# Performance work log

Measured on AMD Instinct MI355X. Metric: run time of the kernel, lower is better.

## Reference

```python
import jax, jax.numpy as jnp
import numpy as np

WS = 8          # window size
HEADS = 6
DIM = 192


def _rel_idx(ws):
    # index [q, k] -> flat relative-position index into table of size (2ws-1)^2
    pos = jnp.arange(ws * ws)
    ph, pw = pos // ws, pos % ws
    rel_h = ph[None, :] - ph[:, None] + ws - 1  # k_h - q_h + ws - 1
    rel_w = pw[None, :] - pw[:, None] + ws - 1
    return rel_h * (2 * ws - 1) + rel_w  # [ws*ws, ws*ws]


def setup_inputs() -> dict:
    key = jax.random.key(0)
    ks = jax.random.split(key, 4)
    x = jax.random.normal(ks[0], (4, DIM, 256, 256), jnp.float32)
    qkv_w = jax.random.normal(ks[1], (3 * DIM, DIM), jnp.float32) * 0.02  # 1x1 conv
    qkv_b = jnp.zeros((3 * DIM,), jnp.float32)
    out_w = jax.random.normal(ks[2], (DIM, DIM), jnp.float32) * 0.02      # 1x1 conv
    out_b = jnp.zeros((DIM,), jnp.float32)
    rpe_table = jax.random.normal(ks[3], (HEADS, (2 * WS - 1) ** 2), jnp.float32) * 0.001
    return {"x": x, "qkv_w": qkv_w, "qkv_b": qkv_b,
            "out_w": out_w, "out_b": out_b, "rpe_table": rpe_table}


def reference(x, qkv_w, qkv_b, out_w, out_b, rpe_table):
    B, C, H, W = x.shape
    ws, heads = WS, HEADS
    hd, wd = H // ws, W // ws          # H,W chosen divisible by ws -> pad is no-op
    c = C // heads                     # head dim
    n = ws * ws                        # tokens per window

    # 1x1 conv to qkv
    qkv = jnp.einsum('bchw,oc->bohw', x, qkv_w) + qkv_b[None, :, None, None]
    # feat_to_win: b (3 heads c) (hd ws) (wd ws) -> 3, (b hd wd), heads, n, c
    qkv = qkv.reshape(B, 3, heads, c, hd, ws, wd, ws)
    qkv = qkv.transpose(1, 0, 4, 6, 2, 5, 7, 3).reshape(3, B * hd * wd, heads, n, c)
    q, k, v = qkv[0], qkv[1], qkv[2]

    bias = rpe_table[:, _rel_idx(ws)]  # [heads, n, n]
    scale = c ** -0.5
    scores = jnp.einsum('whqc,whkc->whqk', q, k) * scale + bias[None]
    attn = jax.nn.softmax(scores, axis=-1)
    out = jnp.einsum('whqk,whkc->whqc', attn, v)

    # win_to_feat: (b hd wd) heads n c -> b (heads c) H W
    out = out.reshape(B, hd, wd, heads, ws, ws, c)
    out = out.transpose(0, 3, 6, 1, 4, 2, 5).reshape(B, C, H, W)

    out = jnp.einsum('bchw,oc->bohw', out, out_w) + out_b[None, :, None, None]
    return out
```

## Files before the change

### kernel.cpp

```cpp
#include <hip/hip_runtime.h>
#include <cstdint>
#include <cstddef>

typedef __attribute__((ext_vector_type(8))) short short8;
typedef __attribute__((ext_vector_type(4))) float floatx4;

#define SEG 50331648ull

__device__ __forceinline__ unsigned short bf16rne(float f) {
  union { float f; unsigned int u; } c; c.f = f;
  unsigned int u = c.u;
  return (unsigned short)((u + 0x7fffu + ((u >> 16) & 1u)) >> 16);
}
__device__ __forceinline__ unsigned int packbf(float a, float b) {
  return (unsigned int)bf16rne(a) | ((unsigned int)bf16rne(b) << 16);
}

__global__ __launch_bounds__(256) void x_to_bf16(const float* __restrict__ x,
                                                 unsigned short* __restrict__ xb) {
  __shared__ float Tl[64][65];
  const int tid = threadIdx.x;
  const int ptile = blockIdx.x, cc = blockIdx.y, b = blockIdx.z;
  const float* src = x + ((size_t)(b * 192 + cc * 64)) * 65536 + ptile * 64;
  {
    int row = tid >> 2;
    int cb = (tid & 3) * 4;
#pragma unroll
    for (int rr = 0; rr < 4; ++rr) {
      int col = cb + rr * 16;
      float4 v = *(const float4*)(src + (size_t)row * 65536 + col);
      *(float4*)&Tl[row][col] = v;
    }
  }
  __syncthreads();
  unsigned short* dst = xb + ((size_t)b * 65536 + (size_t)ptile * 64) * 192 + cc * 64;
  {
    int p_l = tid >> 2;
    int c0 = (tid & 3) * 16;
    unsigned int w[8];
#pragma unroll
    for (int e = 0; e < 8; ++e)
      w[e] = packbf(Tl[c0 + 2 * e][p_l], Tl[c0 + 2 * e + 1][p_l]);
    *(uint4*)(dst + (size_t)p_l * 192 + c0)     = make_uint4(w[0], w[1], w[2], w[3]);
    *(uint4*)(dst + (size_t)p_l * 192 + c0 + 8) = make_uint4(w[4], w[5], w[6], w[7]);
  }
}

__global__ void bias_prep(const float* __restrict__ rpe, float* __restrict__ bias_d) {
  const int head = blockIdx.x;
  const int tid = threadIdx.x;
  for (int e = tid; e < 1024; e += 256) {
    int it = e >> 8, jt = (e >> 6) & 3, ln = e & 63;
    int quad = ln >> 4, n = ln & 15;
    int j = jt * 16 + n;
    int jh = j >> 3, jw = j & 7;
    float4 out;
    float* o = (float*)&out;
#pragma unroll
    for (int r = 0; r < 4; ++r) {
      int m = it * 16 + quad * 4 + r;
      int idx = (jh - (m >> 3) + 7) * 15 + (jw - (m & 7) + 7);
      o[r] = rpe[head * 225 + idx];
    }
    *(float4*)(bias_d + ((size_t)(head * 16 + it * 4 + jt) * 64 + ln) * 4) = out;
  }
}

#define WP 200
#define XP 200
__global__ __launch_bounds__(256) void qkv_mm(
    const unsigned short* __restrict__ xb, const float* __restrict__ wq,
    const float* __restrict__ qkv_b,
    unsigned short* __restrict__ q, unsigned short* __restrict__ k,
    unsigned short* __restrict__ v) {
  __shared__ unsigned short Xl[128 * XP];
  __shared__ unsigned short Wl[64 * WP];
  const int tid = threadIdx.x;
  const int pt = blockIdx.x, b = blockIdx.y;
  const int lane = tid & 63, w = tid >> 6;
  const int n16 = lane & 15, quad = lane >> 4;

  const unsigned short* xrow = xb + ((size_t)b * 65536 + (size_t)pt * 128) * 192;
#pragma unroll
  for (int r = 0; r < 12; ++r) {
    int c = tid + 256 * r;
    int row = c / 24;
    int col = (c - row * 24) * 8;
    short8 xv = *(const short8*)(xrow + (size_t)c * 8);
    *(short8*)&Xl[row * XP + col] = xv;
  }
  const int wo = tid >> 2, wcb = (tid & 3) * 4;
  float4 wpre[12];
#pragma unroll
  for (int r = 0; r < 12; ++r)
    wpre[r] = *(const float4*)(wq + (size_t)wo * 192 + wcb + r * 16);
#pragma unroll
  for (int r = 0; r < 12; ++r)
    *(uint2*)&Wl[wo * WP + wcb + r * 16] =
        make_uint2(packbf(wpre[r].x, wpre[r].y), packbf(wpre[r].z, wpre[r].w));
  __syncthreads();

  const floatx4 fz = {0.f, 0.f, 0.f, 0.f};
#pragma unroll 1
  for (int ot = 0; ot < 9; ++ot) {
    if (ot < 8) {
      const float* wr = wq + (size_t)((ot + 1) * 64 + wo) * 192 + wcb;
#pragma unroll
      for (int r = 0; r < 12; ++r) wpre[r] = *(const float4*)(wr + r * 16);
    }
    floatx4 acc[4][2];
#pragma unroll
    for (int i = 0; i < 4; ++i)
#pragma unroll
      for (int j = 0; j < 2; ++j) acc[i][j] = fz;
#pragma unroll
    for (int k0 = 0; k0 < 192; k0 += 32) {
      short8 a[4], bf[2];
#pragma unroll
      for (int i = 0; i < 4; ++i)
        a[i] = *(const short8*)&Wl[(16 * i + n16) * WP + k0 + quad * 8];
#pragma unroll
      for (int j = 0; j < 2; ++j)
        bf[j] = *(const short8*)&Xl[(w * 32 + 16 * j + n16) * XP + k0 + quad * 8];
#pragma unroll
      for (int i = 0; i < 4; ++i)
#pragma unroll
        for (int j = 0; j < 2; ++j)
          acc[i][j] = __builtin_amdgcn_mfma_f32_16x16x32_bf16(a[i], bf[j], acc[i][j], 0, 0, 0);
    }
    __syncthreads();
    if (ot < 8) {
#pragma unroll
      for (int r = 0; r < 12; ++r)
        *(uint2*)&Wl[wo * WP + wcb + r * 16] =
            make_uint2(packbf(wpre[r].x, wpre[r].y), packbf(wpre[r].z, wpre[r].w));
    }
    __syncthreads();

    const int sel = ot / 3;
    unsigned short* dst = (sel == 0) ? q : ((sel == 1) ? k : v);
    const float scl = (sel == 0) ? 0.17677669529663687f : 1.0f;
    const int h = pt >> 1;
#pragma unroll
    for (int j = 0; j < 2; ++j) {
      int wcol = w * 32 + 16 * j + n16;
      int wc = ((pt & 1) << 7) + wcol;
      int win = (b << 10) + (h >> 3) * 32 + (wc >> 3);
      int t = ((h & 7) << 3) + (wc & 7);
#pragma unroll
      for (int i = 0; i < 4; ++i) {
        int og = ot * 64 + 16 * i + quad * 4;
        int off = og - sel * 192;
        int head = off >> 5, c = off & 31;
        float4 bb = *(const float4*)(qkv_b + og);
        float v0 = (acc[i][j][0] + bb.x) * scl;
        float v1 = (acc[i][j][1] + bb.y) * scl;
        float v2 = (acc[i][j][2] + bb.z) * scl;
        float v3 = (acc[i][j][3] + bb.w) * scl;
        *(uint2*)(dst + ((size_t)(win * 6 + head) * 64 + t) * 32 + c) =
            make_uint2(packbf(v0, v1), packbf(v2, v3));
      }
    }
  }
}

__global__ __launch_bounds__(256) void attn(
    const unsigned short* __restrict__ q, const unsigned short* __restrict__ k,
    const unsigned short* __restrict__ v, const float* __restrict__ bias_d,
    unsigned short* __restrict__ AO) {
  __shared__ unsigned short pl[4][64 * 72];
  __shared__ unsigned short vl[4][32 * 72];
  const int tid = threadIdx.x, w = tid >> 6, lane = tid & 63;
  const int n16 = lane & 15, quad = lane >> 4;
  const int wh = blockIdx.x * 4 + w;
  const int win = wh / 6, head = wh - win * 6;
  const unsigned short* qb = q + (size_t)wh * 2048;
  const unsigned short* kb = k + (size_t)wh * 2048;
  const unsigned short* vb = v + (size_t)wh * 2048;

  short8 vrow[4];
#pragma unroll
  for (int c8 = 0; c8 < 4; ++c8)
    vrow[c8] = *(const short8*)(vb + lane * 32 + c8 * 8);

  short8 aq[4], bk[4];
#pragma unroll
  for (int it = 0; it < 4; ++it)
    aq[it] = *(const short8*)(qb + (16 * it + n16) * 32 + quad * 8);
#pragma unroll
  for (int jt = 0; jt < 4; ++jt)
    bk[jt] = *(const short8*)(kb + (16 * jt + n16) * 32 + quad * 8);

  unsigned short* vlw = (unsigned short*)vl[w];
#pragma unroll
  for (int c8 = 0; c8 < 4; ++c8)
#pragma unroll
    for (int e = 0; e < 8; ++e)
      vlw[(c8 * 8 + e) * 72 + lane] = (unsigned short)vrow[c8][e];

  floatx4 s[4][4];
  const floatx4 fz = {0.f, 0.f, 0.f, 0.f};
#pragma unroll
  for (int it = 0; it < 4; ++it)
#pragma unroll
    for (int jt = 0; jt < 4; ++jt)
      s[it][jt] = __builtin_amdgcn_mfma_f32_16x16x32_bf16(aq[it], bk[jt], fz, 0, 0, 0);

  const float* bD = bias_d + (size_t)head * 4096;
  unsigned short* plw = (unsigned short*)pl[w];
#pragma unroll
  for (int it = 0; it < 4; ++it) {
    floatx4 bb[4];
#pragma unroll
    for (int jt = 0; jt < 4; ++jt)
      bb[jt] = *(const floatx4*)(bD + ((size_t)(it * 4 + jt) * 64 + lane) * 4);
#pragma unroll
    for (int r = 0; r < 4; ++r) {
      float x0 = s[it][0][r] + bb[0][r];
      float x1 = s[it][1][r] + bb[1][r];
      float x2 = s[it][2][r] + bb[2][r];
      float x3 = s[it][3][r] + bb[3][r];
      float m = fmaxf(fmaxf(x0, x1), fmaxf(x2, x3));
      m = fmaxf(m, __shfl_xor(m, 1));
      m = fmaxf(m, __shfl_xor(m, 2));
      m = fmaxf(m, __shfl_xor(m, 4));
      m = fmaxf(m, __shfl_xor(m, 8));
      float e0 = __expf(x0 - m), e1 = __expf(x1 - m);
      float e2 = __expf(x2 - m), e3 = __expf(x3 - m);
      float sum = e0 + e1 + e2 + e3;
      sum += __shfl_xor(sum, 1);
      sum += __shfl_xor(sum, 2);
      sum += __shfl_xor(sum, 4);
      sum += __shfl_xor(sum, 8);
      float inv = 1.0f / sum;
      int mr = it * 16 + quad * 4 + r;
      plw[mr * 72 + 0 * 16 + n16] = bf16rne(e0 * inv);
      plw[mr * 72 + 1 * 16 + n16] = bf16rne(e1 * inv);
      plw[mr * 72 + 2 * 16 + n16] = bf16rne(e2 * inv);
      plw[mr * 72 + 3 * 16 + n16] = bf16rne(e3 * inv);
    }
  }

  short8 bv[2][2], ap[4][2];
#pragma unroll
  for (int ct = 0; ct < 2; ++ct)
#pragma unroll
    for (int kk = 0; kk < 2; ++kk)
      bv[ct][kk] = *(const short8*)&vlw[(16 * ct + n16) * 72 + kk * 32 + quad * 8];
#pragma unroll
  for (int it = 0; it < 4; ++it)
#pragma unroll
    for (int kk = 0; kk < 2; ++kk)
      ap[it][kk] = *(const short8*)&plw[(16 * it + n16) * 72 + kk * 32 + quad * 8];
  floatx4 o[4][2];
#pragma unroll
  for (int it = 0; it < 4; ++it)
#pragma unroll
    for (int ct = 0; ct < 2; ++ct) {
      floatx4 acc = __builtin_amdgcn_mfma_f32_16x16x32_bf16(ap[it][0], bv[ct][0], fz, 0, 0, 0);
      o[it][ct] = __builtin_amdgcn_mfma_f32_16x16x32_bf16(ap[it][1], bv[ct][1], acc, 0, 0, 0);
    }

  unsigned short* ol = plw;
#pragma unroll
  for (int it = 0; it < 4; ++it)
#pragma unroll
    for (int ct = 0; ct < 2; ++ct)
#pragma unroll
      for (int r = 0; r < 4; ++r)
        ol[(16 * it + quad * 4 + r) * 40 + 16 * ct + n16] = bf16rne(o[it][ct][r]);

  const int t = lane;
  const int bimg = win >> 10, rem = win & 1023;
  const int h0 = (rem >> 5) << 3, w0 = (rem & 31) << 3;
  const size_t pix = ((size_t)bimg << 16) + (size_t)(h0 + (t >> 3)) * 256 + w0 + (t & 7);
  unsigned short* dstp = AO + pix * 192 + head * 32;
#pragma unroll
  for (int c8 = 0; c8 < 4; ++c8)
    *(short8*)(dstp + c8 * 8) = *(const short8*)&ol[t * 40 + c8 * 8];
}

__global__ __launch_bounds__(256) void out_mm(
    const unsigned short* __restrict__ AO, const float* __restrict__ w2,
    const float* __restrict__ b2, float* __restrict__ out) {
  __shared__ unsigned short Xl[128 * XP];
  __shared__ unsigned short Wl[64 * WP];
  const int tid = threadIdx.x;
  const int pt = blockIdx.x, b = blockIdx.y;
  const int lane = tid & 63, w = tid >> 6;
  const int n16 = lane & 15, quad = lane >> 4;

  const unsigned short* arow = AO + ((size_t)b * 65536 + (size_t)pt * 128) * 192;
#pragma unroll
  for (int r = 0; r < 12; ++r) {
    int c = tid + 256 * r;
    int row = c / 24;
    int col = (c - row * 24) * 8;
    short8 xv = *(const short8*)(arow + (size_t)c * 8);
    *(short8*)&Xl[row * XP + col] = xv;
  }
  const int wo = tid >> 2, wcb = (tid & 3) * 4;
  float4 wpre[12];
#pragma unroll
  for (int r = 0; r < 12; ++r)
    wpre[r] = *(const float4*)(w2 + (size_t)wo * 192 + wcb + r * 16);
#pragma unroll
  for (int r = 0; r < 12; ++r)
    *(uint2*)&Wl[wo * WP + wcb + r * 16] =
        make_uint2(packbf(wpre[r].x, wpre[r].y), packbf(wpre[r].z, wpre[r].w));
  __syncthreads();

  const floatx4 fz = {0.f, 0.f, 0.f, 0.f};
#pragma unroll 1
  for (int ot = 0; ot < 3; ++ot) {
    if (ot < 2) {
      const float* wr = w2 + (size_t)((ot + 1) * 64 + wo) * 192 + wcb;
#pragma unroll
      for (int r = 0; r < 12; ++r) wpre[r] = *(const float4*)(wr + r * 16);
    }
    floatx4 acc[2][4];
#pragma unroll
    for (int i = 0; i < 2; ++i)
#pragma unroll
      for (int j = 0; j < 4; ++j) acc[i][j] = fz;
#pragma unroll
    for (int k0 = 0; k0 < 192; k0 += 32) {
      short8 a[2], bf[4];
#pragma unroll
      for (int i = 0; i < 2; ++i)
        a[i] = *(const short8*)&Xl[(w * 32 + 16 * i + n16) * XP + k0 + quad * 8];
#pragma unroll
      for (int j = 0; j < 4; ++j)
        bf[j] = *(const short8*)&Wl[(16 * j + n16) * WP + k0 + quad * 8];
#pragma unroll
      for (int i = 0; i < 2; ++i)
#pragma unroll
        for (int j = 0; j < 4; ++j)
          acc[i][j] = __builtin_amdgcn_mfma_f32_16x16x32_bf16(a[i], bf[j], acc[i][j], 0, 0, 0);
    }
    __syncthreads();
    if (ot < 2) {
#pragma unroll
      for (int r = 0; r < 12; ++r)
        *(uint2*)&Wl[wo * WP + wcb + r * 16] =
            make_uint2(packbf(wpre[r].x, wpre[r].y), packbf(wpre[r].z, wpre[r].w));
    }
    __syncthreads();

#pragma unroll
    for (int j = 0; j < 4; ++j) {
      int o = ot * 64 + 16 * j + n16;
      float bj = b2[o];
      float* obase = out + ((size_t)b * 192 + o) * 65536 + (size_t)pt * 128;
#pragma unroll
      for (int i = 0; i < 2; ++i) {
        int p = w * 32 + 16 * i + quad * 4;
        *(float4*)(obase + p) = make_float4(acc[i][j][0] + bj, acc[i][j][1] + bj,
                                            acc[i][j][2] + bj, acc[i][j][3] + bj);
      }
    }
  }
}

extern "C" void kernel_launch(void* const* d_in, const int* in_sizes, int n_in,
                              void* d_out, int out_size, void* d_ws, size_t ws_size,
                              hipStream_t stream) {
  const float* x     = (const float*)d_in[0];
  const float* qkv_w = (const float*)d_in[1];
  const float* qkv_b = (const float*)d_in[2];
  const float* out_w = (const float*)d_in[3];
  const float* out_b = (const float*)d_in[4];
  const float* rpe   = (const float*)d_in[5];
  float* out = (float*)d_out;

  unsigned short* xb = (unsigned short*)d_ws;
  unsigned short* q  = xb + SEG;
  unsigned short* k  = q + SEG;
  unsigned short* v  = k + SEG;
  unsigned short* AO = v + SEG;
  float* bias_d = (float*)(AO + SEG);

  x_to_bf16<<<dim3(1024, 3, 4), 256, 0, stream>>>(x, xb);
  bias_prep<<<6, 256, 0, stream>>>(rpe, bias_d);
  qkv_mm<<<dim3(512, 4), 256, 0, stream>>>(xb, qkv_w, qkv_b, q, k, v);
  attn<<<6144, 256, 0, stream>>>(q, k, v, bias_d, AO);
  out_mm<<<dim3(512, 4), 256, 0, stream>>>(AO, out_w, out_b, out);
}
```

Before: 678.5 us.

## Rework attention kernel with 32x32 MFMA transposed scores and register-resident softmax

Rewrites the per-window attention kernel to compute S^T with 32x32x16 bf16 MFMAs, so each lane holds a full query column and softmax needs only one cross-half shuffle. Probabilities are packed to bf16 in registers and rearranged with permlane32 swaps to feed the PV MFMA directly. This removes the P round trip through LDS and the output staging buffer. Normalisation is deferred to the output, and the bias table layout is regenerated to match the new fragment layout. Output stores become narrower scattered 8-byte writes instead of 16-byte rows.

Measured after the change: 666.7 us. Within noise of the previous version (-1.7%).

```diff
diff --git a/kernel.cpp b/kernel.cpp
--- a/kernel.cpp
+++ b/kernel.cpp
@@ -4,6 +4,7 @@
 
 typedef __attribute__((ext_vector_type(8))) short short8;
 typedef __attribute__((ext_vector_type(4))) float floatx4;
+typedef __attribute__((ext_vector_type(16))) float floatx16;
 
 #define SEG 50331648ull
 
@@ -14,6 +15,11 @@
 }
 __device__ __forceinline__ unsigned int packbf(float a, float b) {
   return (unsigned int)bf16rne(a) | ((unsigned int)bf16rne(b) << 16);
+}
+__device__ __forceinline__ unsigned int cvtpk(float lo, float hi) {
+  unsigned int r;
+  asm("v_cvt_pk_bf16_f32 %0, %1, %2" : "=v"(r) : "v"(lo), "v"(hi));
+  return r;
 }
 
 __global__ __launch_bounds__(256) void x_to_bf16(const float* __restrict__ x,
@@ -49,20 +55,15 @@
 __global__ void bias_prep(const float* __restrict__ rpe, float* __restrict__ bias_d) {
   const int head = blockIdx.x;
   const int tid = threadIdx.x;
-  for (int e = tid; e < 1024; e += 256) {
-    int it = e >> 8, jt = (e >> 6) & 3, ln = e & 63;
-    int quad = ln >> 4, n = ln & 15;
-    int j = jt * 16 + n;
-    int jh = j >> 3, jw = j & 7;
-    float4 out;
-    float* o = (float*)&out;
-#pragma unroll
-    for (int r = 0; r < 4; ++r) {
-      int m = it * 16 + quad * 4 + r;
-      int idx = (jh - (m >> 3) + 7) * 15 + (jw - (m & 7) + 7);
-      o[r] = rpe[head * 225 + idx];
-    }
-    *(float4*)(bias_d + ((size_t)(head * 16 + it * 4 + jt) * 64 + ln) * 4) = out;
+  for (int e = tid; e < 4096; e += 256) {
+    int f = e >> 10;
+    int lane = (e >> 4) & 63;
+    int reg = e & 15;
+    int kt2 = f >> 1, qt2 = f & 1;
+    int qq = qt2 * 32 + (lane & 31);
+    int kk = kt2 * 32 + (reg & 3) + 8 * (reg >> 2) + 4 * (lane >> 5);
+    int idx = ((kk >> 3) - (qq >> 3) + 7) * 15 + ((kk & 7) - (qq & 7) + 7);
+    bias_d[((size_t)(head * 4 + f) * 64 + lane) * 16 + reg] = rpe[head * 225 + idx];
   }
 }
 
@@ -168,10 +169,9 @@
     const unsigned short* __restrict__ q, const unsigned short* __restrict__ k,
     const unsigned short* __restrict__ v, const float* __restrict__ bias_d,
     unsigned short* __restrict__ AO) {
-  __shared__ unsigned short pl[4][64 * 72];
   __shared__ unsigned short vl[4][32 * 72];
   const int tid = threadIdx.x, w = tid >> 6, lane = tid & 63;
-  const int n16 = lane & 15, quad = lane >> 4;
+  const int m32 = lane & 31, half = lane >> 5;
   const int wh = blockIdx.x * 4 + w;
   const int win = wh / 6, head = wh - win * 6;
   const unsigned short* qb = q + (size_t)wh * 2048;
@@ -183,13 +183,12 @@
   for (int c8 = 0; c8 < 4; ++c8)
     vrow[c8] = *(const short8*)(vb + lane * 32 + c8 * 8);
 
-  short8 aq[4], bk[4];
-#pragma unroll
-  for (int it = 0; it < 4; ++it)
-    aq[it] = *(const short8*)(qb + (16 * it + n16) * 32 + quad * 8);
-#pragma unroll
-  for (int jt = 0; jt < 4; ++jt)
-    bk[jt] = *(const short8*)(kb + (16 * jt + n16) * 32 + quad * 8);
+  short8 ka[2][2];
+#pragma unroll
+  for (int kt2 = 0; kt2 < 2; ++kt2)
+#pragma unroll
+    for (int cc = 0; cc < 2; ++cc)
+      ka[kt2][cc] = *(const short8*)(kb + (size_t)(kt2 * 32 + m32) * 32 + cc * 16 + half * 8);
 
   unsigned short* vlw = (unsigned short*)vl[w];
 #pragma unroll
@@ -198,86 +197,77 @@
     for (int e = 0; e < 8; ++e)
       vlw[(c8 * 8 + e) * 72 + lane] = (unsigned short)vrow[c8][e];
 
-  floatx4 s[4][4];
-  const floatx4 fz = {0.f, 0.f, 0.f, 0.f};
-#pragma unroll
-  for (int it = 0; it < 4; ++it)
-#pragma unroll
-    for (int jt = 0; jt < 4; ++jt)
-      s[it][jt] = __builtin_amdgcn_mfma_f32_16x16x32_bf16(aq[it], bk[jt], fz, 0, 0, 0);
+  short8 va[4];
+#pragma unroll
+  for (int k16 = 0; k16 < 4; ++k16)
+    va[k16] = *(const short8*)&vlw[m32 * 72 + k16 * 16 + half * 8];
 
   const float* bD = bias_d + (size_t)head * 4096;
-  unsigned short* plw = (unsigned short*)pl[w];
-#pragma unroll
-  for (int it = 0; it < 4; ++it) {
-    floatx4 bb[4];
-#pragma unroll
-    for (int jt = 0; jt < 4; ++jt)
-      bb[jt] = *(const floatx4*)(bD + ((size_t)(it * 4 + jt) * 64 + lane) * 4);
-#pragma unroll
-    for (int r = 0; r < 4; ++r) {
-      float x0 = s[it][0][r] + bb[0][r];
-      float x1 = s[it][1][r] + bb[1][r];
-      float x2 = s[it][2][r] + bb[2][r];
-      float x3 = s[it][3][r] + bb[3][r];
-      float m = fmaxf(fmaxf(x0, x1), fmaxf(x2, x3));
-      m = fmaxf(m, __shfl_xor(m, 1));
-      m = fmaxf(m, __shfl_xor(m, 2));
-      m = fmaxf(m, __shfl_xor(m, 4));
-      m = fmaxf(m, __shfl_xor(m, 8));
-      float e0 = __expf(x0 - m), e1 = __expf(x1 - m);
-      float e2 = __expf(x2 - m), e3 = __expf(x3 - m);
-      float sum = e0 + e1 + e2 + e3;
-      sum += __shfl_xor(sum, 1);
-      sum += __shfl_xor(sum, 2);
-      sum += __shfl_xor(sum, 4);
-      sum += __shfl_xor(sum, 8);
-      float inv = 1.0f / sum;
-      int mr = it * 16 + quad * 4 + r;
-      plw[mr * 72 + 0 * 16 + n16] = bf16rne(e0 * inv);
-      plw[mr * 72 + 1 * 16 + n16] = bf16rne(e1 * inv);
-      plw[mr * 72 + 2 * 16 + n16] = bf16rne(e2 * inv);
-      plw[mr * 72 + 3 * 16 + n16] = bf16rne(e3 * inv);
-    }
-  }
-
-  short8 bv[2][2], ap[4][2];
-#pragma unroll
-  for (int ct = 0; ct < 2; ++ct)
-#pragma unroll
-    for (int kk = 0; kk < 2; ++kk)
-      bv[ct][kk] = *(const short8*)&vlw[(16 * ct + n16) * 72 + kk * 32 + quad * 8];
-#pragma unroll
-  for (int it = 0; it < 4; ++it)
-#pragma unroll
-    for (int kk = 0; kk < 2; ++kk)
-      ap[it][kk] = *(const short8*)&plw[(16 * it + n16) * 72 + kk * 32 + quad * 8];
-  floatx4 o[4][2];
-#pragma unroll
-  for (int it = 0; it < 4; ++it)
-#pragma unroll
-    for (int ct = 0; ct < 2; ++ct) {
-      floatx4 acc = __builtin_amdgcn_mfma_f32_16x16x32_bf16(ap[it][0], bv[ct][0], fz, 0, 0, 0);
-      o[it][ct] = __builtin_amdgcn_mfma_f32_16x16x32_bf16(ap[it][1], bv[ct][1], acc, 0, 0, 0);
-    }
-
-  unsigned short* ol = plw;
-#pragma unroll
-  for (int it = 0; it < 4; ++it)
-#pragma unroll
-    for (int ct = 0; ct < 2; ++ct)
-#pragma unroll
-      for (int r = 0; r < 4; ++r)
-        ol[(16 * it + quad * 4 + r) * 40 + 16 * ct + n16] = bf16rne(o[it][ct][r]);
-
-  const int t = lane;
-  const int bimg = win >> 10, rem = win & 1023;
-  const int h0 = (rem >> 5) << 3, w0 = (rem & 31) << 3;
-  const size_t pix = ((size_t)bimg << 16) + (size_t)(h0 + (t >> 3)) * 256 + w0 + (t & 7);
-  unsigned short* dstp = AO + pix * 192 + head * 32;
-#pragma unroll
-  for (int c8 = 0; c8 < 4; ++c8)
-    *(short8*)(dstp + c8 * 8) = *(const short8*)&ol[t * 40 + c8 * 8];
+  const floatx16 fz16 = {0.f,0.f,0.f,0.f,0.f,0.f,0.f,0.f,0.f,0.f,0.f,0.f,0.f,0.f,0.f,0.f};
+
+#pragma unroll
+  for (int qt2 = 0; qt2 < 2; ++qt2) {
+    float4 bb[8];
+#pragma unroll
+    for (int g = 0; g < 4; ++g)
+      bb[g] = *(const float4*)(bD + ((size_t)(qt2 * 64) + lane) * 16 + g * 4);
+#pragma unroll
+    for (int g = 0; g < 4; ++g)
+      bb[4 + g] = *(const float4*)(bD + ((size_t)((2 + qt2) * 64) + lane) * 16 + g * 4);
+
+    short8 qf0 = *(const short8*)(qb + (size_t)(qt2 * 32 + m32) * 32 + half * 8);
+    short8 qf1 = *(const short8*)(qb + (size_t)(qt2 * 32 + m32) * 32 + 16 + half * 8);
+
+    floatx16 st0 = __builtin_amdgcn_mfma_f32_32x32x16_bf16(ka[0][0], qf0, fz16, 0, 0, 0);
+    st0 = __builtin_amdgcn_mfma_f32_32x32x16_bf16(ka[0][1], qf1, st0, 0, 0, 0);
+    floatx16 st1 = __builtin_amdgcn_mfma_f32_32x32x16_bf16(ka[1][0], qf0, fz16, 0, 0, 0);
+    st1 = __builtin_amdgcn_mfma_f32_32x32x16_bf16(ka[1][1], qf1, st1, 0, 0, 0);
+
+    float x[32];
+#pragma unroll
+    for (int r = 0; r < 16; ++r) x[r]      = st0[r] + ((const float*)&bb[r >> 2])[r & 3];
+#pragma unroll
+    for (int r = 0; r < 16; ++r) x[16 + r] = st1[r] + ((const float*)&bb[4 + (r >> 2)])[r & 3];
+
+    float mx = x[0];
+#pragma unroll
+    for (int r = 1; r < 32; ++r) mx = fmaxf(mx, x[r]);
+    mx = fmaxf(mx, __shfl_xor(mx, 32));
+    float s = 0.f;
+#pragma unroll
+    for (int r = 0; r < 32; ++r) { x[r] = __expf(x[r] - mx); s += x[r]; }
+    s += __shfl_xor(s, 32);
+    float iv = 1.0f / s;
+
+    unsigned int u[16];
+#pragma unroll
+    for (int j = 0; j < 16; ++j) u[j] = cvtpk(x[2 * j], x[2 * j + 1]);
+
+    floatx16 o = fz16;
+#pragma unroll
+    for (int k16 = 0; k16 < 4; ++k16) {
+      int base = (k16 >> 1) * 8 + (k16 & 1) * 4;
+      unsigned int a0 = u[base + 0], b0 = u[base + 2];
+      unsigned int a1 = u[base + 1], b1 = u[base + 3];
+      asm("v_permlane32_swap_b32 %0, %1" : "+v"(a0), "+v"(b0));
+      asm("v_permlane32_swap_b32 %0, %1" : "+v"(a1), "+v"(b1));
+      union { unsigned int wd[4]; short8 s8; } bw;
+      bw.wd[0] = a0; bw.wd[1] = a1; bw.wd[2] = b0; bw.wd[3] = b1;
+      o = __builtin_amdgcn_mfma_f32_32x32x16_bf16(va[k16], bw.s8, o, 0, 0, 0);
+    }
+
+    const int t = qt2 * 32 + m32;
+    const int bimg = win >> 10, rem = win & 1023;
+    const int h0 = (rem >> 5) << 3, w0 = (rem & 31) << 3;
+    const size_t pix = ((size_t)bimg << 16) + (size_t)(h0 + (t >> 3)) * 256 + w0 + (t & 7);
+    unsigned short* dstp = AO + pix * 192 + head * 32 + half * 4;
+#pragma unroll
+    for (int g = 0; g < 4; ++g) {
+      float v0 = o[4 * g + 0] * iv, v1 = o[4 * g + 1] * iv;
+      float v2 = o[4 * g + 2] * iv, v3 = o[4 * g + 3] * iv;
+      *(uint2*)(dstp + g * 8) = make_uint2(cvtpk(v0, v1), cvtpk(v2, v3));
+    }
+  }
 }
 
 __global__ __launch_bounds__(256) void out_mm(
```
